# Performance work log

Measured on AMD Instinct MI355X. Metric: run time of the kernel, lower is better.

## Reference

```python
import jax, jax.numpy as jnp
import numpy as np

B, N, D, H = 8, 2048, 512, 8  # batch, seq (incl. CLS), emb_dim, heads


def setup_inputs() -> dict:
    key = jax.random.key(0)
    kx, km, k1, k2, k3, k4 = jax.random.split(key, 6)
    x = jax.random.normal(kx, (B, N, D), dtype=jnp.float32)
    # mask covers the N-1 non-CLS tokens; forward pads a leading True for CLS
    mask = jax.random.bernoulli(km, p=0.9, shape=(B, N - 1))
    s = 0.02
    Wqkv = jax.random.normal(k1, (D, 3 * D), dtype=jnp.float32) * s
    bqkv = jax.random.normal(k2, (3 * D,), dtype=jnp.float32) * s
    Wout = jax.random.normal(k3, (D, D), dtype=jnp.float32) * s
    bout = jax.random.normal(k4, (D,), dtype=jnp.float32) * s
    return {"x": x, "mask": mask, "Wqkv": Wqkv, "bqkv": bqkv,
            "Wout": Wout, "bout": bout, "num_heads": H}


def reference(x, mask, Wqkv, bqkv, Wout, bout, num_heads):
    b, n, d = x.shape
    h = num_heads
    dh = d // h
    scale = d ** (-0.5)  # NOTE: module scales by emb_dim^-0.5, not head_dim^-0.5

    qkv = x @ Wqkv + bqkv                      # [b, n, 3d]
    q, k, v = jnp.split(qkv, 3, axis=-1)
    def to_heads(t):
        return t.reshape(b, n, h, dh).transpose(0, 2, 1, 3)  # [b, h, n, dh]
    q, k, v = map(to_heads, (q, k, v))

    scores = jnp.einsum('bhqd,bhkd->bhqk', q, k) * scale     # [b, h, n, n]

    # pad leading True for CLS token, then outer-product pair mask
    m = jnp.pad(mask, ((0, 0), (1, 0)), constant_values=True)  # [b, n]
    pair = m[:, None, :, None] & m[:, None, None, :]           # [b, 1, n, n]
    neg = jnp.asarray(-1e9, dtype=scores.dtype)  # finite stand-in for -inf (avoids NaN rows)
    scores = jnp.where(pair, scores, neg)

    attn = jax.nn.softmax(scores, axis=-1)
    out = jnp.einsum('bhqk,bhkd->bhqd', attn, v)               # [b, h, n, dh]
    out = out.transpose(0, 2, 1, 3).reshape(b, n, d)
    return out @ Wout + bout
```

## Files before the change

### kernel.cpp

```cpp
#include <hip/hip_runtime.h>
#include <math.h>

#define BB  8
#define SEQ 2048
#define EMB 512
#define NH  8
#define DH  64
#define NBH (BB * NH)
#define MROWS (BB * SEQ)
#define QKV_ELEMS ((size_t)NBH * SEQ * DH)
#define MASK_ELEMS (BB * (SEQ - 1))
#define QSCALE 0.06375871307545f

typedef __attribute__((ext_vector_type(8)))  short short8;
typedef __attribute__((ext_vector_type(4)))  float float4e;
typedef __attribute__((ext_vector_type(16))) float float16e;
typedef __attribute__((ext_vector_type(4)))  unsigned int uint4e;
typedef __attribute__((ext_vector_type(2)))  unsigned int uint2e;
typedef unsigned short ushort_t;

static __device__ inline unsigned short f2bf(float f) {
    unsigned int u = __float_as_uint(f);
    unsigned int r = (u + 0x7fffu + ((u >> 16) & 1u)) >> 16;
    return (unsigned short)r;
}

static __device__ inline void gl_lds16(const unsigned short* g, unsigned short* l) {
    __builtin_amdgcn_global_load_lds(
        (const __attribute__((address_space(1))) void*)g,
        (__attribute__((address_space(3))) void*)l, 16, 0, 0);
}

#define PREP_CONV   8192
#define PREP_MASK   (PREP_CONV + 64)
#define PREP_WQ     (PREP_MASK + (1536 / 32) * (EMB / 32))
#define PREP_TOTAL  (PREP_WQ + (EMB / 32) * (EMB / 32))

__global__ __launch_bounds__(256) void prep(const float* __restrict__ x,
                                            const void* __restrict__ mraw,
                                            const float* __restrict__ Wqkv,
                                            const float* __restrict__ Wout,
                                            ushort_t* __restrict__ xb,
                                            float* __restrict__ pmf,
                                            ushort_t* __restrict__ wqt,
                                            ushort_t* __restrict__ wot) {
    __shared__ float T[32][33];
    __shared__ int flag;
    const int bid = blockIdx.x;
    const int tid = threadIdx.x;

    if (bid < PREP_CONV) {
        const size_t i = ((size_t)bid * 256 + tid) * 4;
        float4 v = *(const float4*)&x[i];
        ushort4 o;
        o.x = f2bf(v.x); o.y = f2bf(v.y); o.z = f2bf(v.z); o.w = f2bf(v.w);
        *(ushort4*)&xb[i] = o;
    } else if (bid < PREP_MASK) {
        if (tid == 0) flag = 0;
        __syncthreads();
        const unsigned int* mi = (const unsigned int*)mraw;
        int local = 0;
        for (int i = tid; i < MASK_ELEMS / 4; i += 256) {
            if (mi[i] > 1u) local = 1;
        }
        if (local) flag = 1;
        __syncthreads();
        const int isbyte = flag;
        const unsigned char* mb = (const unsigned char*)mraw;
        const int* m32 = (const int*)mraw;
        const int i = (bid - PREP_CONV) * 256 + tid;
        const int b = i >> 11, n = i & (SEQ - 1);
        int v;
        if (n == 0) v = 1;
        else {
            const int src = b * (SEQ - 1) + n - 1;
            v = isbyte ? (int)mb[src] : (m32[src] != 0 ? 1 : 0);
        }
        pmf[i] = v ? 1.0f : 0.0f;
    } else {
        const float* src;
        ushort_t* dst;
        int N, idx;
        if (bid < PREP_WQ) {
            src = Wqkv; dst = wqt; N = 1536; idx = bid - PREP_MASK;
        } else {
            src = Wout; dst = wot; N = EMB; idx = bid - PREP_WQ;
        }
        const int nb = N / 32;
        const int n0 = (idx % nb) * 32;
        const int k0 = (idx / nb) * 32;
        {
            const int r = tid >> 3, c4 = (tid & 7) * 4;
            *(float4*)&T[r][c4] = *(const float4*)&src[(size_t)(k0 + r) * N + n0 + c4];
        }
        __syncthreads();
        const int n = tid >> 3, k4 = (tid & 7) * 4;
        ushort4 hv;
        hv.x = f2bf(T[k4 + 0][n]);
        hv.y = f2bf(T[k4 + 1][n]);
        hv.z = f2bf(T[k4 + 2][n]);
        hv.w = f2bf(T[k4 + 3][n]);
        *(ushort4*)&dst[(size_t)(n0 + n) * EMB + k0 + k4] = hv;
    }
}

__global__ __launch_bounds__(256) void qkv_mfma(const ushort_t* __restrict__ xb,
                                                const ushort_t* __restrict__ wt,
                                                const float* __restrict__ bias,
                                                ushort_t* __restrict__ qb,
                                                ushort_t* __restrict__ kb,
                                                ushort_t* __restrict__ vt) {
    __shared__ __align__(16) ushort_t As[128 * 32];
    __shared__ __align__(16) ushort_t Bs[128 * 32];
    const int tid  = threadIdx.x;
    const int w    = tid >> 6;
    const int lane = tid & 63;
    const int l16  = lane & 15;
    const int quad = lane >> 4;
    const int wq   = w >> 1;
    const int wn   = w & 1;
    const int row0 = blockIdx.y * 128;
    const int col0 = blockIdx.x * 128;

    float4e acc[4][4];
    #pragma unroll
    for (int i = 0; i < 4; ++i)
        #pragma unroll
        for (int j = 0; j < 4; ++j) acc[i][j] = (float4e){0.f, 0.f, 0.f, 0.f};

    const int srow = tid >> 2;
    const int csrc = (tid & 3) ^ (srow & 3);

    for (int k0 = 0; k0 < EMB; k0 += 32) {
        #pragma unroll
        for (int s = 0; s < 2; ++s) {
            const int row = s * 64 + srow;
            gl_lds16(xb + (size_t)(row0 + row) * EMB + k0 + csrc * 8,
                     As + s * 2048 + w * 512);
            gl_lds16(wt + (size_t)(col0 + row) * EMB + k0 + csrc * 8,
                     Bs + s * 2048 + w * 512);
        }
        __syncthreads();
        short8 af[4], bf[4];
        #pragma unroll
        for (int mt = 0; mt < 4; ++mt) {
            const int rm = wq * 64 + mt * 16 + l16;
            af[mt] = *(const short8*)(As + rm * 32 + ((quad ^ (rm & 3)) * 8));
        }
        #pragma unroll
        for (int nt = 0; nt < 4; ++nt) {
            const int rn = wn * 64 + nt * 16 + l16;
            bf[nt] = *(const short8*)(Bs + rn * 32 + ((quad ^ (rn & 3)) * 8));
        }
        #pragma unroll
        for (int mt = 0; mt < 4; ++mt)
            #pragma unroll
            for (int nt = 0; nt < 4; ++nt)
                acc[mt][nt] = __builtin_amdgcn_mfma_f32_16x16x32_bf16(af[mt], bf[nt], acc[mt][nt], 0, 0, 0);
        __syncthreads();
    }

    #pragma unroll
    for (int nt = 0; nt < 4; ++nt) {
        const int cb    = col0 + wn * 64 + nt * 16;
        const int which = cb >> 9;
        const int h     = (cb >> 6) & 7;
        const int dcol  = (cb & 63) + l16;
        const float bz  = bias[cb + l16];
        if (which == 2) {
            #pragma unroll
            for (int mt = 0; mt < 4; ++mt) {
                const int rg = row0 + wq * 64 + mt * 16 + quad * 4;
                const int b = rg >> 11, n = rg & (SEQ - 1);
                ushort4 ov;
                ov.x = f2bf(acc[mt][nt][0] + bz);
                ov.y = f2bf(acc[mt][nt][1] + bz);
                ov.z = f2bf(acc[mt][nt][2] + bz);
                ov.w = f2bf(acc[mt][nt][3] + bz);
                *(ushort4*)&vt[((size_t)(b * NH + h) * DH + dcol) * SEQ + n] = ov;
            }
        } else {
            ushort_t* base = (which == 0) ? qb : kb;
            const float sc = (which == 0) ? QSCALE : 1.0f;
            #pragma unroll
            for (int mt = 0; mt < 4; ++mt) {
                #pragma unroll
                for (int i = 0; i < 4; ++i) {
                    const int rg = row0 + wq * 64 + mt * 16 + quad * 4 + i;
                    const int b = rg >> 11;
                    const int n = rg & (SEQ - 1);
                    base[((size_t)(b * NH + h) * SEQ + n) * DH + dcol] =
                        f2bf((acc[mt][nt][i] + bz) * sc);
                }
            }
        }
    }
}

__device__ inline void stage_tile(const ushort_t* kbh, const ushort_t* vbh, int kt,
                                  ushort_t* Kd, ushort_t* Vd,
                                  const int* crow, const int* csoff, int wbase) {
    #pragma unroll
    for (int j = 0; j < 2; ++j) {
        gl_lds16(kbh + (size_t)(kt * 64 + crow[j]) * DH + csoff[j],
                 Kd + (j * 256 + wbase) * 8);
        gl_lds16(vbh + (size_t)crow[j] * SEQ + kt * 64 + csoff[j],
                 Vd + (j * 256 + wbase) * 8);
    }
}

__global__ __launch_bounds__(256, 4) void attn_mfma(const ushort_t* __restrict__ qb,
                                                    const ushort_t* __restrict__ kb,
                                                    const ushort_t* __restrict__ vt,
                                                    const float* __restrict__ pmf,
                                                    ushort_t* __restrict__ ab) {
    __shared__ __align__(16) ushort_t Ks[2][64 * 64];
    __shared__ __align__(16) ushort_t Vts[2][64 * 64];
    __shared__ float lw[4][32];

    const int tid = threadIdx.x;
    const int w   = tid >> 6;
    const int lane = tid & 63;
    const int l5  = lane & 31;
    const int h   = lane >> 5;
    const int bid = blockIdx.x;
    const int ord = bid >> 3;
    const int bh  = (bid & 7) * 8 + (ord >> 4);
    const int qt  = ord & 15;
    const int b   = bh >> 3;
    const int hh  = bh & 7;
    const int q0  = qt * 128 + w * 32;

    const ushort_t* qbh = qb + (size_t)bh * SEQ * DH;
    short8 qf[4];
    #pragma unroll
    for (int kc = 0; kc < 4; ++kc)
        qf[kc] = *(const short8*)(qbh + (size_t)(q0 + l5) * DH + kc * 16 + h * 8);

    const float mq  = pmf[b * SEQ + q0 + l5];
    const float fnq = 1.0f - mq;

    int crow[2], csoff[2];
    #pragma unroll
    for (int j = 0; j < 2; ++j) {
        const int c = j * 256 + tid;
        crow[j]  = c >> 3;
        csoff[j] = ((c & 7) ^ (crow[j] & 7)) * 8;
    }
    const int wbase = w * 64;
    const ushort_t* kbh = kb + (size_t)bh * SEQ * DH;
    const ushort_t* vbh = vt + (size_t)bh * DH * SEQ;
    const float*    mrow = pmf + b * SEQ;

    float16e o[2];
    o[0] = (float16e)0.0f;
    o[1] = (float16e)0.0f;
    float l_i = 0.f;

    stage_tile(kbh, vbh, 0, Ks[0], Vts[0], crow, csoff, wbase);

    for (int kt = 0; kt < 32; ++kt) {
        __syncthreads();
        const int cur = kt & 1;
        if (kt < 31)
            stage_tile(kbh, vbh, kt + 1, Ks[cur ^ 1], Vts[cur ^ 1], crow, csoff, wbase);

        #pragma unroll
        for (int s = 0; s < 2; ++s) {
            float4e m4[4];
            #pragma unroll
            for (int g2 = 0; g2 < 4; ++g2) {
                const float4e raw = *(const float4e*)(mrow + kt * 64 + s * 32 + g2 * 8 + h * 4);
                m4[g2] = raw * mq;
            }

            const int krow = s * 32 + l5;
            short8 kf[4];
            #pragma unroll
            for (int kc = 0; kc < 4; ++kc)
                kf[kc] = *(const short8*)(Ks[cur] + krow * 64 + (((kc * 2 + h) ^ (krow & 7)) * 8));
            float16e st = (float16e)0.0f;
            __builtin_amdgcn_s_setprio(1);
            #pragma unroll
            for (int kc = 0; kc < 4; ++kc)
                st = __builtin_amdgcn_mfma_f32_32x32x16_bf16(kf[kc], qf[kc], st, 0, 0, 0);
            __builtin_amdgcn_s_setprio(0);

            unsigned int a[8];
            float lacc = 0.f;
            #pragma unroll
            for (int j = 0; j < 8; ++j) {
                const float mk0 = m4[j >> 1][(2 * j) & 3];
                const float mk1 = m4[j >> 1][(2 * j + 1) & 3];
                const float p0 = fmaf(__builtin_amdgcn_exp2f(st[2 * j]),     mk0, fnq);
                const float p1 = fmaf(__builtin_amdgcn_exp2f(st[2 * j + 1]), mk1, fnq);
                lacc += p0 + p1;
                a[j] = (__float_as_uint(p0) >> 16) | (__float_as_uint(p1) & 0xffff0000u);
            }
            l_i += lacc;

            short8 af[2];
            #pragma unroll
            for (int c = 0; c < 2; ++c) {
                const uint2e r02 = __builtin_amdgcn_permlane32_swap(a[4 * c],     a[4 * c + 2], false, false);
                const uint2e r13 = __builtin_amdgcn_permlane32_swap(a[4 * c + 1], a[4 * c + 3], false, false);
                uint4e fv;
                fv.x = r02[0];
                fv.y = r13[0];
                fv.z = r02[1];
                fv.w = r13[1];
                af[c] = __builtin_bit_cast(short8, fv);
            }

            __builtin_amdgcn_s_setprio(1);
            #pragma unroll
            for (int c = 0; c < 2; ++c) {
                #pragma unroll
                for (int d = 0; d < 2; ++d) {
                    const int vrow = d * 32 + l5;
                    const short8 vf = *(const short8*)(Vts[cur] + vrow * 64 +
                                       (((s * 4 + c * 2 + h) ^ (vrow & 7)) * 8));
                    o[d] = __builtin_amdgcn_mfma_f32_32x32x16_bf16(af[c], vf, o[d], 0, 0, 0);
                }
            }
            __builtin_amdgcn_s_setprio(0);
        }
    }

    {
        const float l = l_i + __shfl_xor(l_i, 32);
        lw[w][l5] = l;
    }

    ushort_t* ob = ab + ((size_t)b * SEQ + q0) * EMB + hh * DH;
    #pragma unroll
    for (int r = 0; r < 16; ++r) {
        const int ql = (r & 3) + 8 * (r >> 2) + 4 * h;
        const float inv = 1.0f / lw[w][ql];
        #pragma unroll
        for (int d = 0; d < 2; ++d)
            ob[(size_t)ql * EMB + d * 32 + l5] = f2bf(o[d][r] * inv);
    }
}

__global__ __launch_bounds__(256) void out_mfma(const ushort_t* __restrict__ ab,
                                                const ushort_t* __restrict__ wot,
                                                const float* __restrict__ bias,
                                                float* __restrict__ out) {
    __shared__ __align__(16) ushort_t As[128 * 32];
    __shared__ __align__(16) ushort_t Bs[128 * 32];
    const int tid  = threadIdx.x;
    const int w    = tid >> 6;
    const int lane = tid & 63;
    const int l16  = lane & 15;
    const int quad = lane >> 4;
    const int wq   = w >> 1;
    const int wn   = w & 1;
    const int row0 = blockIdx.y * 128;
    const int col0 = blockIdx.x * 128;

    float4e acc[4][4];
    #pragma unroll
    for (int i = 0; i < 4; ++i)
        #pragma unroll
        for (int j = 0; j < 4; ++j) acc[i][j] = (float4e){0.f, 0.f, 0.f, 0.f};

    const int srow = tid >> 2;
    const int csrc = (tid & 3) ^ (srow & 3);

    for (int k0 = 0; k0 < EMB; k0 += 32) {
        #pragma unroll
        for (int s = 0; s < 2; ++s) {
            const int row = s * 64 + srow;
            gl_lds16(ab + (size_t)(row0 + row) * EMB + k0 + csrc * 8,
                     As + s * 2048 + w * 512);
            gl_lds16(wot + (size_t)(col0 + row) * EMB + k0 + csrc * 8,
                     Bs + s * 2048 + w * 512);
        }
        __syncthreads();
        short8 af[4], bf[4];
        #pragma unroll
        for (int mt = 0; mt < 4; ++mt) {
            const int rm = wq * 64 + mt * 16 + l16;
            af[mt] = *(const short8*)(As + rm * 32 + ((quad ^ (rm & 3)) * 8));
        }
        #pragma unroll
        for (int nt = 0; nt < 4; ++nt) {
            const int rn = wn * 64 + nt * 16 + l16;
            bf[nt] = *(const short8*)(Bs + rn * 32 + ((quad ^ (rn & 3)) * 8));
        }
        #pragma unroll
        for (int mt = 0; mt < 4; ++mt)
            #pragma unroll
            for (int nt = 0; nt < 4; ++nt)
                acc[mt][nt] = __builtin_amdgcn_mfma_f32_16x16x32_bf16(af[mt], bf[nt], acc[mt][nt], 0, 0, 0);
        __syncthreads();
    }

    #pragma unroll
    for (int nt = 0; nt < 4; ++nt) {
        const int col_g = col0 + wn * 64 + nt * 16 + l16;
        const float bz = bias[col_g];
        #pragma unroll
        for (int mt = 0; mt < 4; ++mt) {
            #pragma unroll
            for (int i = 0; i < 4; ++i) {
                const int row_g = row0 + wq * 64 + mt * 16 + quad * 4 + i;
                out[(size_t)row_g * EMB + col_g] = acc[mt][nt][i] + bz;
            }
        }
    }
}

extern "C" void kernel_launch(void* const* d_in, const int* in_sizes, int n_in,
                              void* d_out, int out_size, void* d_ws, size_t ws_size,
                              hipStream_t stream) {
    const float* x    = (const float*)d_in[0];
    const void*  mask = d_in[1];
    const float* Wqkv = (const float*)d_in[2];
    const float* bqkv = (const float*)d_in[3];
    const float* Wout = (const float*)d_in[4];
    const float* bout = (const float*)d_in[5];
    float* out = (float*)d_out;

    ushort_t* xb  = (ushort_t*)d_ws;
    ushort_t* wqt = xb + (size_t)MROWS * EMB;
    ushort_t* wot = wqt + (size_t)1536 * EMB;
    ushort_t* qb  = wot + (size_t)EMB * EMB;
    ushort_t* kb  = qb + QKV_ELEMS;
    ushort_t* vt  = kb + QKV_ELEMS;
    ushort_t* ab  = vt + QKV_ELEMS;
    float*    pmf = (float*)(ab + (size_t)MROWS * EMB);

    prep<<<dim3(PREP_TOTAL), 256, 0, stream>>>(x, mask, Wqkv, Wout, xb, pmf, wqt, wot);
    qkv_mfma<<<dim3(1536 / 128, MROWS / 128), 256, 0, stream>>>(xb, wqt, bqkv, qb, kb, vt);
    attn_mfma<<<dim3(NBH * (SEQ / 128)), 256, 0, stream>>>(qb, kb, vt, pmf, ab);
    out_mfma<<<dim3(EMB / 128, MROWS / 128), 256, 0, stream>>>(ab, wot, bout, out);
}
```

Measured before the change: 258.1 us.

## Load K and V fragments directly from global memory in attention kernel

Removes the LDS double-buffered staging of K and V tiles and the per-tile block barrier. Each single-wave block now reads its K and V MFMA fragments straight from global memory, relying on L1/L2 caching, and the grid becomes one 32-query wave per block. This drops the sync and LDS traffic, but each wave now fetches K/V on its own instead of sharing tiles across four waves. Global load latency also sits directly in front of the MFMAs with no prefetch.

```diff
diff --git a/kernel.cpp b/kernel.cpp
--- a/kernel.cpp
+++ b/kernel.cpp
@@ -197,39 +197,23 @@
     }
 }
 
-__device__ inline void stage_tile(const ushort_t* kbh, const ushort_t* vbh, int kt,
-                                  ushort_t* Kd, ushort_t* Vd,
-                                  const int* crow, const int* csoff, int wbase) {
-    #pragma unroll
-    for (int j = 0; j < 2; ++j) {
-        gl_lds16(kbh + (size_t)(kt * 64 + crow[j]) * DH + csoff[j],
-                 Kd + (j * 256 + wbase) * 8);
-        gl_lds16(vbh + (size_t)crow[j] * SEQ + kt * 64 + csoff[j],
-                 Vd + (j * 256 + wbase) * 8);
-    }
-}
-
-__global__ __launch_bounds__(256, 4) void attn_mfma(const ushort_t* __restrict__ qb,
-                                                    const ushort_t* __restrict__ kb,
-                                                    const ushort_t* __restrict__ vt,
-                                                    const float* __restrict__ pmf,
-                                                    ushort_t* __restrict__ ab) {
-    __shared__ __align__(16) ushort_t Ks[2][64 * 64];
-    __shared__ __align__(16) ushort_t Vts[2][64 * 64];
-    __shared__ float lw[4][32];
-
-    const int tid = threadIdx.x;
-    const int w   = tid >> 6;
-    const int lane = tid & 63;
-    const int l5  = lane & 31;
-    const int h   = lane >> 5;
+__global__ __launch_bounds__(64, 4) void attn_mfma(const ushort_t* __restrict__ qb,
+                                                   const ushort_t* __restrict__ kb,
+                                                   const ushort_t* __restrict__ vt,
+                                                   const float* __restrict__ pmf,
+                                                   ushort_t* __restrict__ ab) {
+    __shared__ float lw[32];
+
+    const int lane = threadIdx.x;
+    const int l5   = lane & 31;
+    const int h    = lane >> 5;
     const int bid = blockIdx.x;
     const int ord = bid >> 3;
-    const int bh  = (bid & 7) * 8 + (ord >> 4);
-    const int qt  = ord & 15;
+    const int bh  = (bid & 7) * 8 + (ord >> 6);
+    const int qt  = ord & 63;
     const int b   = bh >> 3;
     const int hh  = bh & 7;
-    const int q0  = qt * 128 + w * 32;
+    const int q0  = qt * 32;
 
     const ushort_t* qbh = qb + (size_t)bh * SEQ * DH;
     short8 qf[4];
@@ -240,14 +224,6 @@
     const float mq  = pmf[b * SEQ + q0 + l5];
     const float fnq = 1.0f - mq;
 
-    int crow[2], csoff[2];
-    #pragma unroll
-    for (int j = 0; j < 2; ++j) {
-        const int c = j * 256 + tid;
-        crow[j]  = c >> 3;
-        csoff[j] = ((c & 7) ^ (crow[j] & 7)) * 8;
-    }
-    const int wbase = w * 64;
     const ushort_t* kbh = kb + (size_t)bh * SEQ * DH;
     const ushort_t* vbh = vt + (size_t)bh * DH * SEQ;
     const float*    mrow = pmf + b * SEQ;
@@ -257,14 +233,7 @@
     o[1] = (float16e)0.0f;
     float l_i = 0.f;
 
-    stage_tile(kbh, vbh, 0, Ks[0], Vts[0], crow, csoff, wbase);
-
     for (int kt = 0; kt < 32; ++kt) {
-        __syncthreads();
-        const int cur = kt & 1;
-        if (kt < 31)
-            stage_tile(kbh, vbh, kt + 1, Ks[cur ^ 1], Vts[cur ^ 1], crow, csoff, wbase);
-
         #pragma unroll
         for (int s = 0; s < 2; ++s) {
             float4e m4[4];
@@ -274,11 +243,10 @@
                 m4[g2] = raw * mq;
             }
 
-            const int krow = s * 32 + l5;
             short8 kf[4];
             #pragma unroll
             for (int kc = 0; kc < 4; ++kc)
-                kf[kc] = *(const short8*)(Ks[cur] + krow * 64 + (((kc * 2 + h) ^ (krow & 7)) * 8));
+                kf[kc] = *(const short8*)(kbh + (size_t)(kt * 64 + s * 32 + l5) * DH + kc * 16 + h * 8);
             float16e st = (float16e)0.0f;
             __builtin_amdgcn_s_setprio(1);
             #pragma unroll
@@ -312,31 +280,33 @@
                 af[c] = __builtin_bit_cast(short8, fv);
             }
 
+            short8 vf[2][2];
+            #pragma unroll
+            for (int c = 0; c < 2; ++c)
+                #pragma unroll
+                for (int d = 0; d < 2; ++d)
+                    vf[c][d] = *(const short8*)(vbh + (size_t)(d * 32 + l5) * SEQ +
+                                                kt * 64 + (s * 4 + c * 2 + h) * 8);
             __builtin_amdgcn_s_setprio(1);
             #pragma unroll
-            for (int c = 0; c < 2; ++c) {
+            for (int c = 0; c < 2; ++c)
                 #pragma unroll
-                for (int d = 0; d < 2; ++d) {
-                    const int vrow = d * 32 + l5;
-                    const short8 vf = *(const short8*)(Vts[cur] + vrow * 64 +
-                                       (((s * 4 + c * 2 + h) ^ (vrow & 7)) * 8));
-                    o[d] = __builtin_amdgcn_mfma_f32_32x32x16_bf16(af[c], vf, o[d], 0, 0, 0);
-                }
-            }
+                for (int d = 0; d < 2; ++d)
+                    o[d] = __builtin_amdgcn_mfma_f32_32x32x16_bf16(af[c], vf[c][d], o[d], 0, 0, 0);
             __builtin_amdgcn_s_setprio(0);
         }
     }
 
     {
         const float l = l_i + __shfl_xor(l_i, 32);
-        lw[w][l5] = l;
+        lw[l5] = l;
     }
 
     ushort_t* ob = ab + ((size_t)b * SEQ + q0) * EMB + hh * DH;
     #pragma unroll
     for (int r = 0; r < 16; ++r) {
         const int ql = (r & 3) + 8 * (r >> 2) + 4 * h;
-        const float inv = 1.0f / lw[w][ql];
+        const float inv = 1.0f / lw[ql];
         #pragma unroll
         for (int d = 0; d < 2; ++d)
             ob[(size_t)ql * EMB + d * 32 + l5] = f2bf(o[d][r] * inv);
@@ -434,6 +404,6 @@
 
     prep<<<dim3(PREP_TOTAL), 256, 0, stream>>>(x, mask, Wqkv, Wout, xb, pmf, wqt, wot);
     qkv_mfma<<<dim3(1536 / 128, MROWS / 128), 256, 0, stream>>>(xb, wqt, bqkv, qb, kb, vt);
-    attn_mfma<<<dim3(NBH * (SEQ / 128)), 256, 0, stream>>>(qb, kb, vt, pmf, ab);
+    attn_mfma<<<dim3(NBH * (SEQ / 32)), 64, 0, stream>>>(qb, kb, vt, pmf, ab);
     out_mfma<<<dim3(EMB / 128, MROWS / 128), 256, 0, stream>>>(ab, wot, bout, out);
 }
```

After: 417.2 us. 61.7% more time.
